# Optimization experiments

Hardware: AMD Instinct MI355X
Metric: run time of the kernel (lower is better)

Reference implementation:

```python
import jax, jax.numpy as jnp
import numpy as np

SEQ_LEN = 256  # seq_len from init_kwargs
HIDDEN = 1024


def setup_inputs() -> dict:
    key = jax.random.key(0)
    k1, k2, k3, k4, k5 = jax.random.split(key, 5)
    I, H = 512, HIDDEN
    s = 1.0 / np.sqrt(H)  # torch LSTMCell init scale (uniform); normal*s is fine for a numeric baseline
    return {
        "context_vector": jax.random.normal(k1, (256, I), dtype=jnp.float32),
        "w_ih": jax.random.normal(k2, (4 * H, I), dtype=jnp.float32) * s,
        "w_hh": jax.random.normal(k3, (4 * H, H), dtype=jnp.float32) * s,
        "b_ih": jax.random.normal(k4, (4 * H,), dtype=jnp.float32) * s,
        "b_hh": jax.random.normal(k5, (4 * H,), dtype=jnp.float32) * s,
    }


def reference(context_vector, w_ih, w_hh, b_ih, b_hh):
    # Input at every timestep is the same context vector -> precompute the
    # input-hidden projection once (the fusion a custom kernel would do).
    bs = context_vector.shape[0]
    H = w_hh.shape[1]
    x_proj = context_vector @ w_ih.T + b_ih + b_hh  # (bs, 4H)

    def step(carry, _):
        h, c = carry
        gates = x_proj + h @ w_hh.T  # (bs, 4H)
        i, f, g, o = jnp.split(gates, 4, axis=-1)  # torch gate order: i, f, g, o
        i = jax.nn.sigmoid(i)
        f = jax.nn.sigmoid(f)
        g = jnp.tanh(g)
        o = jax.nn.sigmoid(o)
        c_new = f * c + i * g
        h_new = o * jnp.tanh(c_new)
        return (h_new, c_new), h_new

    zeros = jnp.zeros((bs, H), dtype=context_vector.dtype)
    (_, _), hs = jax.lax.scan(step, (zeros, zeros), None, length=SEQ_LEN)
    return jnp.transpose(hs, (1, 0, 2))  # (bs, T, H)
```

## Files before the change

### kernel.cpp

```cpp
#include <hip/hip_runtime.h>
#include <math.h>


typedef _Float16 fp16_t;
typedef _Float16 f16x8 __attribute__((ext_vector_type(8)));
typedef float    f32x4 __attribute__((ext_vector_type(4)));

#define HID   1024
#define SEQ   256
#define INF   512
#define PF    8

#define CTR_STRIDE_U32 32

#define MFMA(a, b, c) __builtin_amdgcn_mfma_f32_16x16x32_f16((a), (b), (c), 0, 0, 0)

__device__ __forceinline__ float sigm(float x) { return 1.0f / (1.0f + __expf(-x)); }
__device__ __forceinline__ float tanh_fast(float x) { return 1.0f - 2.0f / (__expf(2.0f * x) + 1.0f); }

__device__ __forceinline__ f16x8 cvt8(float4 lo, float4 hi) {
    f16x8 v;
    v[0] = (fp16_t)lo.x; v[1] = (fp16_t)lo.y; v[2] = (fp16_t)lo.z; v[3] = (fp16_t)lo.w;
    v[4] = (fp16_t)hi.x; v[5] = (fp16_t)hi.y; v[6] = (fp16_t)hi.z; v[7] = (fp16_t)hi.w;
    return v;
}

__global__ __launch_bounds__(256, 1) void lstm_persist_f16(
    const float* __restrict__ ctx,
    const float* __restrict__ wih,
    const float* __restrict__ whh,
    const float* __restrict__ bih,
    const float* __restrict__ bhh,
    float* __restrict__ out,
    unsigned int* __restrict__ ctrs,
    fp16_t* __restrict__ hbuf,
    const int tmask, const int do_fence)
{
    __shared__ __align__(16) fp16_t wlds[32 * HID];

    const int tid  = threadIdx.x;
    const int lane = tid & 63;
    const int wid  = tid >> 6;
    const int bid  = blockIdx.x;
    const int mg   = bid & 1;
    const int ng   = bid >> 1;
    const int cl   = lane & 15;
    const int q    = lane >> 4;
    const int hi   = (cl >> 3) & 1;
    const int nx   = cl & 7;
    const int rot  = ng & 31;
    const int odd  = lane & 1;

    unsigned int* my_ctr   = ctrs + (((mg << 4) + (ng & 15)) * CTR_STRIDE_U32);
    unsigned int* poll_ctr = ctrs + (((mg << 4) + (lane & 15)) * CTR_STRIDE_U32);

    for (int Gi = tid; Gi < 32 * 128; Gi += 256) {
        const int n = Gi >> 7, g = Gi & 127;
        const int grow = ((n >> 3) << 10) + (ng << 3) + (n & 7);
        const float4* src = reinterpret_cast<const float4*>(whh + (size_t)grow * HID + g * 8);
        float4 u0 = src[0], u1 = src[1];
        reinterpret_cast<f16x8*>(wlds)[n * 128 + (g ^ (n & 7))] = cvt8(u0, u1);
    }

    const int rowA0 = mg * 128 + wid * 32 + cl;
    const int rowA1 = rowA0 + 16;
    const int n0 = cl, n1 = 16 + cl;
    const int grow0 = ((n0 >> 3) << 10) + (ng << 3) + (n0 & 7);
    const int grow1 = ((n1 >> 3) << 10) + (ng << 3) + (n1 & 7);

    f32x4 x00 = {0.f, 0.f, 0.f, 0.f}, x01 = x00, x10 = x00, x11 = x00;
    {
        const float4* ca0 = reinterpret_cast<const float4*>(ctx + (size_t)rowA0 * INF);
        const float4* ca1 = reinterpret_cast<const float4*>(ctx + (size_t)rowA1 * INF);
        const float4* wb0 = reinterpret_cast<const float4*>(wih + (size_t)grow0 * INF);
        const float4* wb1 = reinterpret_cast<const float4*>(wih + (size_t)grow1 * INF);
#pragma unroll 4
        for (int kb = 0; kb < 16; ++kb) {
            const int vi = kb * 8 + q * 2;
            f16x8 a0 = cvt8(ca0[vi], ca0[vi + 1]);
            f16x8 a1 = cvt8(ca1[vi], ca1[vi + 1]);
            f16x8 b0 = cvt8(wb0[vi], wb0[vi + 1]);
            f16x8 b1 = cvt8(wb1[vi], wb1[vi + 1]);
            x00 = MFMA(a0, b0, x00); x01 = MFMA(a0, b1, x01);
            x10 = MFMA(a1, b0, x10); x11 = MFMA(a1, b1, x11);
        }
        const float bias0 = bih[grow0] + bhh[grow0];
        const float bias1 = bih[grow1] + bhh[grow1];
#pragma unroll
        for (int r = 0; r < 4; ++r) {
            x00[r] += bias0; x10[r] += bias0;
            x01[r] += bias1; x11[r] += bias1;
        }
    }
    __syncthreads();

    const f16x8* wv = reinterpret_cast<const f16x8*>(wlds);

    const int sampW = mg * 128 + wid * 32 + hi * 16 + q * 4;
    const int ug    = (ng << 3) + (cl & 7);

    f32x4 cst = {0.f, 0.f, 0.f, 0.f};

    for (int t = 0; t < SEQ; ++t) {
        f32x4 a00 = x00, a01 = x01, a10 = x10, a11 = x11;

        if (t > 0) {
            if (wid == 0) {
                const unsigned tgt = (unsigned)(8 * t);
                for (int spin = 0; spin < (1 << 22); ++spin) {
                    unsigned c = __hip_atomic_load(poll_ctr, __ATOMIC_RELAXED, __HIP_MEMORY_SCOPE_AGENT);
                    if (__all(c >= tgt)) break;
                    __builtin_amdgcn_s_sleep(1);
                }
                if (do_fence)
                    __builtin_amdgcn_fence(__ATOMIC_ACQUIRE, "agent");
            }
            __syncthreads();
            asm volatile("" ::: "memory");

            const size_t pbase = (size_t)(((t - 1) & tmask) * 256);
            const f16x8* pa0 = reinterpret_cast<const f16x8*>(hbuf + ((pbase + rowA0) << 10));
            const f16x8* pa1 = reinterpret_cast<const f16x8*>(hbuf + ((pbase + rowA1) << 10));

            f16x8 va0[PF], va1[PF];
#pragma unroll
            for (int i = 0; i < PF; ++i) {
                const int k = (i + rot) & 31;
                va0[i] = pa0[k * 4 + q];
                va1[i] = pa1[k * 4 + q];
            }
#pragma unroll
            for (int kb = 0; kb < 32; ++kb) {
                const int s = kb & (PF - 1);
                f16x8 A0 = va0[s], A1 = va1[s];
                if (kb < 32 - PF) {
                    const int k = (kb + PF + rot) & 31;
                    va0[s] = pa0[k * 4 + q];
                    va1[s] = pa1[k * 4 + q];
                }
                const int cur = (kb + rot) & 31;
                const int gs = ((cur << 2) + q) ^ nx;
                f16x8 vb0 = wv[(cl << 7) + gs];
                f16x8 vb1 = wv[(cl << 7) + gs + 2048];
                a00 = MFMA(A0, vb0, a00); a01 = MFMA(A0, vb1, a01);
                a10 = MFMA(A1, vb0, a10); a11 = MFMA(A1, vb1, a11);
            }
        }

        f32x4 e00, e01, e10, e11;
#pragma unroll
        for (int r = 0; r < 4; ++r) {
            e00[r] = __shfl_xor(a00[r], 8, 64);
            e01[r] = __shfl_xor(a01[r], 8, 64);
            e10[r] = __shfl_xor(a10[r], 8, 64);
            e11[r] = __shfl_xor(a11[r], 8, 64);
        }
        f32x4 iv = hi ? e10 : a00;
        f32x4 fv = hi ? a10 : e00;
        f32x4 gv = hi ? e11 : a01;
        f32x4 ov = hi ? a11 : e01;

        float    hhf[4];
        unsigned hu[4];
#pragma unroll
        for (int r = 0; r < 4; ++r) {
            float ii = sigm(iv[r]);
            float ff = sigm(fv[r]);
            float gg = tanh_fast(gv[r]);
            float oo = sigm(ov[r]);
            float cc = ff * cst[r] + ii * gg;
            cst[r] = cc;
            float hh = oo * tanh_fast(cc);
            hhf[r] = hh;
            fp16_t hf = (fp16_t)hh;
            hu[r] = (unsigned)__builtin_bit_cast(unsigned short, hf);
        }

        unsigned pd0, pd1, pd2, pd3;
        {
            unsigned pu;
            pu = __shfl_xor(hu[0], 1, 64); pd0 = odd ? (pu | (hu[0] << 16)) : (hu[0] | (pu << 16));
            pu = __shfl_xor(hu[1], 1, 64); pd1 = odd ? (pu | (hu[1] << 16)) : (hu[1] | (pu << 16));
            pu = __shfl_xor(hu[2], 1, 64); pd2 = odd ? (pu | (hu[2] << 16)) : (hu[2] | (pu << 16));
            pu = __shfl_xor(hu[3], 1, 64); pd3 = odd ? (pu | (hu[3] << 16)) : (hu[3] | (pu << 16));
        }
        const int rq = lane & 3;
        unsigned pdr = (rq & 2) ? ((rq & 1) ? pd3 : pd2) : ((rq & 1) ? pd1 : pd0);
        unsigned pdx = (rq & 2) ? ((rq & 1) ? pd1 : pd0) : ((rq & 1) ? pd3 : pd2);
        unsigned qdr = __shfl_xor(pdx, 2, 64);
        unsigned long long u64 = (lane & 2)
            ? (((unsigned long long)pdr << 32) | (unsigned long long)qdr)
            : (((unsigned long long)qdr << 32) | (unsigned long long)pdr);
        fp16_t* hbw = hbuf + (((size_t)((t & tmask) * 256 + sampW + rq)) << 10) + (ug & ~3);
        __hip_atomic_exchange(reinterpret_cast<unsigned long long*>(hbw), u64,
                              __ATOMIC_RELAXED, __HIP_MEMORY_SCOPE_AGENT);

        __syncthreads();
        if (tid == 0)
            __hip_atomic_fetch_add(my_ctr, 1u,
                                   __ATOMIC_RELAXED, __HIP_MEMORY_SCOPE_AGENT);

        float* op = out + ((size_t)sampW * SEQ + t) * HID + ug;
#pragma unroll
        for (int r = 0; r < 4; ++r)
            __builtin_nontemporal_store(hhf[r], op + (size_t)r * SEQ * HID);
    }
}

__global__ __launch_bounds__(256, 1) void lstm_persist_f32(
    const float* __restrict__ ctx,
    const float* __restrict__ wih,
    const float* __restrict__ whh,
    const float* __restrict__ bih,
    const float* __restrict__ bhh,
    float* __restrict__ out,
    unsigned int* __restrict__ flags)
{
    __shared__ __align__(16) fp16_t wlds[32 * HID];

    const int tid  = threadIdx.x;
    const int lane = tid & 63;
    const int wid  = tid >> 6;
    const int bid  = blockIdx.x;
    const int mg   = bid >> 7;
    const int ng   = bid & 127;
    const int cl   = lane & 15;
    const int q    = lane >> 4;
    const int hi   = (cl >> 3) & 1;
    const int nx   = cl & 7;
    const int rot  = ng & 31;

    for (int Gi = tid; Gi < 32 * 128; Gi += 256) {
        const int n = Gi >> 7, g = Gi & 127;
        const int grow = ((n >> 3) << 10) + (ng << 3) + (n & 7);
        const float4* src = reinterpret_cast<const float4*>(whh + (size_t)grow * HID + g * 8);
        float4 u0 = src[0], u1 = src[1];
        reinterpret_cast<f16x8*>(wlds)[n * 128 + (g ^ (n & 7))] = cvt8(u0, u1);
    }

    const int rowA0 = mg * 128 + wid * 32 + cl;
    const int rowA1 = rowA0 + 16;
    const int n0 = cl, n1 = 16 + cl;
    const int grow0 = ((n0 >> 3) << 10) + (ng << 3) + (n0 & 7);
    const int grow1 = ((n1 >> 3) << 10) + (ng << 3) + (n1 & 7);

    f32x4 x00 = {0.f, 0.f, 0.f, 0.f}, x01 = x00, x10 = x00, x11 = x00;
    {
        const float4* ca0 = reinterpret_cast<const float4*>(ctx + (size_t)rowA0 * INF);
        const float4* ca1 = reinterpret_cast<const float4*>(ctx + (size_t)rowA1 * INF);
        const float4* wb0 = reinterpret_cast<const float4*>(wih + (size_t)grow0 * INF);
        const float4* wb1 = reinterpret_cast<const float4*>(wih + (size_t)grow1 * INF);
#pragma unroll 4
        for (int kb = 0; kb < 16; ++kb) {
            const int vi = kb * 8 + q * 2;
            f16x8 a0 = cvt8(ca0[vi], ca0[vi + 1]);
            f16x8 a1 = cvt8(ca1[vi], ca1[vi + 1]);
            f16x8 b0 = cvt8(wb0[vi], wb0[vi + 1]);
            f16x8 b1 = cvt8(wb1[vi], wb1[vi + 1]);
            x00 = MFMA(a0, b0, x00); x01 = MFMA(a0, b1, x01);
            x10 = MFMA(a1, b0, x10); x11 = MFMA(a1, b1, x11);
        }
        const float bias0 = bih[grow0] + bhh[grow0];
        const float bias1 = bih[grow1] + bhh[grow1];
#pragma unroll
        for (int r = 0; r < 4; ++r) {
            x00[r] += bias0; x10[r] += bias0;
            x01[r] += bias1; x11[r] += bias1;
        }
    }
    __syncthreads();

    const f16x8* wv = reinterpret_cast<const f16x8*>(wlds);
    const int sampW = mg * 128 + wid * 32 + hi * 16 + q * 4;
    const int ug    = (ng << 3) + (cl & 7);

    f32x4 cst = {0.f, 0.f, 0.f, 0.f};

    for (int t = 0; t < SEQ; ++t) {
        f32x4 a00 = x00, a01 = x01, a10 = x10, a11 = x11;

        if (t > 0) {
            if (wid == 0) {
                const unsigned tgt = (unsigned)t;
                const unsigned* fb = flags + mg * 128;
                for (;;) {
                    unsigned f0 = __hip_atomic_load(fb + lane,      __ATOMIC_RELAXED, __HIP_MEMORY_SCOPE_AGENT);
                    unsigned f1 = __hip_atomic_load(fb + 64 + lane, __ATOMIC_RELAXED, __HIP_MEMORY_SCOPE_AGENT);
                    if (__all((f0 >= tgt) && (f1 >= tgt))) break;
                    __builtin_amdgcn_s_sleep(1);
                }
            }
            __syncthreads();
            asm volatile("" ::: "memory");

            const float4* pa0 = reinterpret_cast<const float4*>(out + ((size_t)rowA0 * SEQ + (t - 1)) * HID);
            const float4* pa1 = reinterpret_cast<const float4*>(out + ((size_t)rowA1 * SEQ + (t - 1)) * HID);

            int cur = rot;
            float4 c00 = pa0[cur * 8 + q * 2], c01 = pa0[cur * 8 + q * 2 + 1];
            float4 c10 = pa1[cur * 8 + q * 2], c11 = pa1[cur * 8 + q * 2 + 1];
#pragma unroll 8
            for (int kb = 0; kb < 32; ++kb) {
                float4 d00, d01, d10, d11;
                if (kb < 31) {
                    const int nxt = (kb + 1 + rot) & 31;
                    d00 = pa0[nxt * 8 + q * 2]; d01 = pa0[nxt * 8 + q * 2 + 1];
                    d10 = pa1[nxt * 8 + q * 2]; d11 = pa1[nxt * 8 + q * 2 + 1];
                }
                f16x8 va0 = cvt8(c00, c01);
                f16x8 va1 = cvt8(c10, c11);
                const int gs = ((cur << 2) + q) ^ nx;
                f16x8 vb0 = wv[(cl << 7) + gs];
                f16x8 vb1 = wv[(cl << 7) + gs + 2048];
                a00 = MFMA(va0, vb0, a00); a01 = MFMA(va0, vb1, a01);
                a10 = MFMA(va1, vb0, a10); a11 = MFMA(va1, vb1, a11);
                c00 = d00; c01 = d01; c10 = d10; c11 = d11;
                cur = (kb + 1 + rot) & 31;
            }
        }

        f32x4 e00, e01, e10, e11;
#pragma unroll
        for (int r = 0; r < 4; ++r) {
            e00[r] = __shfl_xor(a00[r], 8, 64);
            e01[r] = __shfl_xor(a01[r], 8, 64);
            e10[r] = __shfl_xor(a10[r], 8, 64);
            e11[r] = __shfl_xor(a11[r], 8, 64);
        }
        f32x4 iv = hi ? e10 : a00;
        f32x4 fv = hi ? a10 : e00;
        f32x4 gv = hi ? e11 : a01;
        f32x4 ov = hi ? a11 : e01;

        unsigned* ow = reinterpret_cast<unsigned*>(out + ((size_t)sampW * SEQ + t) * HID + ug);
#pragma unroll
        for (int r = 0; r < 4; ++r) {
            float ii = sigm(iv[r]);
            float ff = sigm(fv[r]);
            float gg = tanh_fast(gv[r]);
            float oo = sigm(ov[r]);
            float cc = ff * cst[r] + ii * gg;
            cst[r] = cc;
            float hh = oo * tanh_fast(cc);
            __hip_atomic_exchange(ow + (size_t)r * SEQ * HID,
                                  __builtin_bit_cast(unsigned, hh),
                                  __ATOMIC_RELAXED, __HIP_MEMORY_SCOPE_AGENT);
        }

        __syncthreads();
        if (tid == 0)
            __hip_atomic_exchange(&flags[bid], (unsigned)(t + 1),
                                  __ATOMIC_RELAXED, __HIP_MEMORY_SCOPE_AGENT);
    }
}

extern "C" void kernel_launch(void* const* d_in, const int* in_sizes, int n_in,
                              void* d_out, int out_size, void* d_ws, size_t ws_size,
                              hipStream_t stream) {
    const float* ctx = (const float*)d_in[0];
    const float* wih = (const float*)d_in[1];
    const float* whh = (const float*)d_in[2];
    const float* bih = (const float*)d_in[3];
    const float* bhh = (const float*)d_in[4];
    float* out = (float*)d_out;

    const size_t need_once   = 8192 + (size_t)SEQ * 256 * 1024 * sizeof(fp16_t);
    const size_t need_parity = 8192 + (size_t)2   * 256 * 1024 * sizeof(fp16_t);

    if (ws_size >= need_once) {
        unsigned int* ctrs = (unsigned int*)d_ws;
        fp16_t* hbuf = (fp16_t*)((char*)d_ws + 8192);
        hipMemsetAsync(d_ws, 0, 8192, stream);
        lstm_persist_f16<<<dim3(256), dim3(256), 0, stream>>>(
            ctx, wih, whh, bih, bhh, out, ctrs, hbuf, SEQ - 1, 0);
    } else if (ws_size >= need_parity) {
        unsigned int* ctrs = (unsigned int*)d_ws;
        fp16_t* hbuf = (fp16_t*)((char*)d_ws + 8192);
        hipMemsetAsync(d_ws, 0, 8192, stream);
        lstm_persist_f16<<<dim3(256), dim3(256), 0, stream>>>(
            ctx, wih, whh, bih, bhh, out, ctrs, hbuf, 1, 1);
    } else {
        unsigned int* flags = (unsigned int*)d_ws;
        hipMemsetAsync(d_ws, 0, 1024, stream);
        lstm_persist_f32<<<dim3(256), dim3(256), 0, stream>>>(
            ctx, wih, whh, bih, bhh, out, flags);
    }
}
```

Measured before the change: 2.775 ms.

## Merge both batch halves into one 512-thread block sharing LDS weights

Adds a persistent LSTM kernel variant that launches 128 blocks of 512 threads instead of 256 blocks of 256. In each block, the two 4-wave groups handle the two batch halves for the same hidden-unit slice, so the block loads its W_hh slice into LDS once and reuses it for both halves. The goal is to halve the number of blocks in the cross-block step synchronisation and to avoid converting the W_hh slice twice. In exchange, each CU carries twice the MFMA work per step. The two halves are also tied together by block barriers, and the spin-wait gives up after a shorter timeout through a new alive flag, with no acquire fence.

```diff
diff --git a/kernel.cpp b/kernel.cpp
--- a/kernel.cpp
+++ b/kernel.cpp
@@ -25,7 +25,7 @@
     return v;
 }
 
-__global__ __launch_bounds__(256, 1) void lstm_persist_f16(
+__global__ __launch_bounds__(512, 1) void lstm_persist_dual(
     const float* __restrict__ ctx,
     const float* __restrict__ wih,
     const float* __restrict__ whh,
@@ -33,17 +33,16 @@
     const float* __restrict__ bhh,
     float* __restrict__ out,
     unsigned int* __restrict__ ctrs,
-    fp16_t* __restrict__ hbuf,
-    const int tmask, const int do_fence)
+    fp16_t* __restrict__ hbuf)
 {
     __shared__ __align__(16) fp16_t wlds[32 * HID];
 
     const int tid  = threadIdx.x;
     const int lane = tid & 63;
     const int wid  = tid >> 6;
-    const int bid  = blockIdx.x;
-    const int mg   = bid & 1;
-    const int ng   = bid >> 1;
+    const int w4   = wid & 3;
+    const int mg   = wid >> 2;
+    const int ng   = blockIdx.x;
     const int cl   = lane & 15;
     const int q    = lane >> 4;
     const int hi   = (cl >> 3) & 1;
@@ -54,7 +53,7 @@
     unsigned int* my_ctr   = ctrs + (((mg << 4) + (ng & 15)) * CTR_STRIDE_U32);
     unsigned int* poll_ctr = ctrs + (((mg << 4) + (lane & 15)) * CTR_STRIDE_U32);
 
-    for (int Gi = tid; Gi < 32 * 128; Gi += 256) {
+    for (int Gi = tid; Gi < 32 * 128; Gi += 512) {
         const int n = Gi >> 7, g = Gi & 127;
         const int grow = ((n >> 3) << 10) + (ng << 3) + (n & 7);
         const float4* src = reinterpret_cast<const float4*>(whh + (size_t)grow * HID + g * 8);
@@ -62,7 +61,7 @@
         reinterpret_cast<f16x8*>(wlds)[n * 128 + (g ^ (n & 7))] = cvt8(u0, u1);
     }
 
-    const int rowA0 = mg * 128 + wid * 32 + cl;
+    const int rowA0 = mg * 128 + w4 * 32 + cl;
     const int rowA1 = rowA0 + 16;
     const int n0 = cl, n1 = 16 + cl;
     const int grow0 = ((n0 >> 3) << 10) + (ng << 3) + (n0 & 7);
@@ -96,6 +95,184 @@
 
     const f16x8* wv = reinterpret_cast<const f16x8*>(wlds);
 
+    const int sampW = mg * 128 + w4 * 32 + hi * 16 + q * 4;
+    const int ug    = (ng << 3) + (cl & 7);
+
+    f32x4 cst = {0.f, 0.f, 0.f, 0.f};
+    int alive = 1;
+
+    for (int t = 0; t < SEQ; ++t) {
+        f32x4 a00 = x00, a01 = x01, a10 = x10, a11 = x11;
+
+        if (t > 0) {
+            if (w4 == 0 && alive) {
+                const unsigned tgt = (unsigned)(8 * t);
+                int spin = 0;
+                for (; spin < (1 << 20); ++spin) {
+                    unsigned c = __hip_atomic_load(poll_ctr, __ATOMIC_RELAXED, __HIP_MEMORY_SCOPE_AGENT);
+                    if (__all(c >= tgt)) break;
+                    __builtin_amdgcn_s_sleep(1);
+                }
+                if (spin >= (1 << 20)) alive = 0;
+            }
+            __syncthreads();
+            asm volatile("" ::: "memory");
+
+            const size_t pbase = (size_t)(t - 1) * 256;
+            const f16x8* pa0 = reinterpret_cast<const f16x8*>(hbuf + ((pbase + rowA0) << 10));
+            const f16x8* pa1 = reinterpret_cast<const f16x8*>(hbuf + ((pbase + rowA1) << 10));
+
+            f16x8 va0[PF], va1[PF];
+#pragma unroll
+            for (int i = 0; i < PF; ++i) {
+                const int k = (i + rot) & 31;
+                va0[i] = pa0[k * 4 + q];
+                va1[i] = pa1[k * 4 + q];
+            }
+#pragma unroll
+            for (int kb = 0; kb < 32; ++kb) {
+                const int s = kb & (PF - 1);
+                f16x8 A0 = va0[s], A1 = va1[s];
+                if (kb < 32 - PF) {
+                    const int k = (kb + PF + rot) & 31;
+                    va0[s] = pa0[k * 4 + q];
+                    va1[s] = pa1[k * 4 + q];
+                }
+                const int cur = (kb + rot) & 31;
+                const int gs = ((cur << 2) + q) ^ nx;
+                f16x8 vb0 = wv[(cl << 7) + gs];
+                f16x8 vb1 = wv[(cl << 7) + gs + 2048];
+                a00 = MFMA(A0, vb0, a00); a01 = MFMA(A0, vb1, a01);
+                a10 = MFMA(A1, vb0, a10); a11 = MFMA(A1, vb1, a11);
+            }
+        }
+
+        f32x4 e00, e01, e10, e11;
+#pragma unroll
+        for (int r = 0; r < 4; ++r) {
+            e00[r] = __shfl_xor(a00[r], 8, 64);
+            e01[r] = __shfl_xor(a01[r], 8, 64);
+            e10[r] = __shfl_xor(a10[r], 8, 64);
+            e11[r] = __shfl_xor(a11[r], 8, 64);
+        }
+        f32x4 iv = hi ? e10 : a00;
+        f32x4 fv = hi ? a10 : e00;
+        f32x4 gv = hi ? e11 : a01;
+        f32x4 ov = hi ? a11 : e01;
+
+        float    hhf[4];
+        unsigned hu[4];
+#pragma unroll
+        for (int r = 0; r < 4; ++r) {
+            float ii = sigm(iv[r]);
+            float ff = sigm(fv[r]);
+            float gg = tanh_fast(gv[r]);
+            float oo = sigm(ov[r]);
+            float cc = ff * cst[r] + ii * gg;
+            cst[r] = cc;
+            float hh = oo * tanh_fast(cc);
+            hhf[r] = hh;
+            fp16_t hf = (fp16_t)hh;
+            hu[r] = (unsigned)__builtin_bit_cast(unsigned short, hf);
+        }
+
+        unsigned pd0, pd1, pd2, pd3;
+        {
+            unsigned pu;
+            pu = __shfl_xor(hu[0], 1, 64); pd0 = odd ? (pu | (hu[0] << 16)) : (hu[0] | (pu << 16));
+            pu = __shfl_xor(hu[1], 1, 64); pd1 = odd ? (pu | (hu[1] << 16)) : (hu[1] | (pu << 16));
+            pu = __shfl_xor(hu[2], 1, 64); pd2 = odd ? (pu | (hu[2] << 16)) : (hu[2] | (pu << 16));
+            pu = __shfl_xor(hu[3], 1, 64); pd3 = odd ? (pu | (hu[3] << 16)) : (hu[3] | (pu << 16));
+        }
+        const int rq = lane & 3;
+        unsigned pdr = (rq & 2) ? ((rq & 1) ? pd3 : pd2) : ((rq & 1) ? pd1 : pd0);
+        unsigned pdx = (rq & 2) ? ((rq & 1) ? pd1 : pd0) : ((rq & 1) ? pd3 : pd2);
+        unsigned qdr = __shfl_xor(pdx, 2, 64);
+        unsigned long long u64 = (lane & 2)
+            ? (((unsigned long long)pdr << 32) | (unsigned long long)qdr)
+            : (((unsigned long long)qdr << 32) | (unsigned long long)pdr);
+        fp16_t* hbw = hbuf + (((size_t)((size_t)t * 256 + sampW + rq)) << 10) + (ug & ~3);
+        __hip_atomic_exchange(reinterpret_cast<unsigned long long*>(hbw), u64,
+                              __ATOMIC_RELAXED, __HIP_MEMORY_SCOPE_AGENT);
+
+        __syncthreads();
+        if ((tid & 255) == 0)
+            __hip_atomic_fetch_add(my_ctr, 1u,
+                                   __ATOMIC_RELAXED, __HIP_MEMORY_SCOPE_AGENT);
+
+        float* op = out + ((size_t)sampW * SEQ + t) * HID + ug;
+#pragma unroll
+        for (int r = 0; r < 4; ++r)
+            __builtin_nontemporal_store(hhf[r], op + (size_t)r * SEQ * HID);
+    }
+}
+
+__global__ __launch_bounds__(256, 1) void lstm_persist_f16(
+    const float* __restrict__ ctx, const float* __restrict__ wih,
+    const float* __restrict__ whh, const float* __restrict__ bih,
+    const float* __restrict__ bhh, float* __restrict__ out,
+    unsigned int* __restrict__ ctrs, fp16_t* __restrict__ hbuf,
+    const int tmask, const int do_fence)
+{
+    __shared__ __align__(16) fp16_t wlds[32 * HID];
+
+    const int tid  = threadIdx.x;
+    const int lane = tid & 63;
+    const int wid  = tid >> 6;
+    const int bid  = blockIdx.x;
+    const int mg   = bid & 1;
+    const int ng   = bid >> 1;
+    const int cl   = lane & 15;
+    const int q    = lane >> 4;
+    const int hi   = (cl >> 3) & 1;
+    const int nx   = cl & 7;
+    const int rot  = ng & 31;
+    const int odd  = lane & 1;
+
+    unsigned int* my_ctr   = ctrs + (((mg << 4) + (ng & 15)) * CTR_STRIDE_U32);
+    unsigned int* poll_ctr = ctrs + (((mg << 4) + (lane & 15)) * CTR_STRIDE_U32);
+
+    for (int Gi = tid; Gi < 32 * 128; Gi += 256) {
+        const int n = Gi >> 7, g = Gi & 127;
+        const int grow = ((n >> 3) << 10) + (ng << 3) + (n & 7);
+        const float4* src = reinterpret_cast<const float4*>(whh + (size_t)grow * HID + g * 8);
+        float4 u0 = src[0], u1 = src[1];
+        reinterpret_cast<f16x8*>(wlds)[n * 128 + (g ^ (n & 7))] = cvt8(u0, u1);
+    }
+
+    const int rowA0 = mg * 128 + wid * 32 + cl;
+    const int rowA1 = rowA0 + 16;
+    const int n0 = cl, n1 = 16 + cl;
+    const int grow0 = ((n0 >> 3) << 10) + (ng << 3) + (n0 & 7);
+    const int grow1 = ((n1 >> 3) << 10) + (ng << 3) + (n1 & 7);
+
+    f32x4 x00 = {0.f, 0.f, 0.f, 0.f}, x01 = x00, x10 = x00, x11 = x00;
+    {
+        const float4* ca0 = reinterpret_cast<const float4*>(ctx + (size_t)rowA0 * INF);
+        const float4* ca1 = reinterpret_cast<const float4*>(ctx + (size_t)rowA1 * INF);
+        const float4* wb0 = reinterpret_cast<const float4*>(wih + (size_t)grow0 * INF);
+        const float4* wb1 = reinterpret_cast<const float4*>(wih + (size_t)grow1 * INF);
+#pragma unroll 4
+        for (int kb = 0; kb < 16; ++kb) {
+            const int vi = kb * 8 + q * 2;
+            f16x8 a0 = cvt8(ca0[vi], ca0[vi + 1]);
+            f16x8 a1 = cvt8(ca1[vi], ca1[vi + 1]);
+            f16x8 b0 = cvt8(wb0[vi], wb0[vi + 1]);
+            f16x8 b1 = cvt8(wb1[vi], wb1[vi + 1]);
+            x00 = MFMA(a0, b0, x00); x01 = MFMA(a0, b1, x01);
+            x10 = MFMA(a1, b0, x10); x11 = MFMA(a1, b1, x11);
+        }
+        const float bias0 = bih[grow0] + bhh[grow0];
+        const float bias1 = bih[grow1] + bhh[grow1];
+#pragma unroll
+        for (int r = 0; r < 4; ++r) {
+            x00[r] += bias0; x10[r] += bias0;
+            x01[r] += bias1; x11[r] += bias1;
+        }
+    }
+    __syncthreads();
+
+    const f16x8* wv = reinterpret_cast<const f16x8*>(wlds);
     const int sampW = mg * 128 + wid * 32 + hi * 16 + q * 4;
     const int ug    = (ng << 3) + (cl & 7);
 
@@ -107,7 +284,7 @@
         if (t > 0) {
             if (wid == 0) {
                 const unsigned tgt = (unsigned)(8 * t);
-                for (int spin = 0; spin < (1 << 22); ++spin) {
+                for (int spin = 0; spin < (1 << 20); ++spin) {
                     unsigned c = __hip_atomic_load(poll_ctr, __ATOMIC_RELAXED, __HIP_MEMORY_SCOPE_AGENT);
                     if (__all(c >= tgt)) break;
                     __builtin_amdgcn_s_sleep(1);
@@ -371,8 +548,8 @@
         unsigned int* ctrs = (unsigned int*)d_ws;
         fp16_t* hbuf = (fp16_t*)((char*)d_ws + 8192);
         hipMemsetAsync(d_ws, 0, 8192, stream);
-        lstm_persist_f16<<<dim3(256), dim3(256), 0, stream>>>(
-            ctx, wih, whh, bih, bhh, out, ctrs, hbuf, SEQ - 1, 0);
+        lstm_persist_dual<<<dim3(128), dim3(512), 0, stream>>>(
+            ctx, wih, whh, bih, bhh, out, ctrs, hbuf);
     } else if (ws_size >= need_parity) {
         unsigned int* ctrs = (unsigned int*)d_ws;
         fp16_t* hbuf = (fp16_t*)((char*)d_ws + 8192);
```

After: 4.591 ms. 65.4% more time.
